# Optimization experiments

Measured on AMD Instinct MI355X. Metric: run time of the kernel, lower is better.

## Reference

```python
import jax, jax.numpy as jnp
import numpy as np

D_MODEL = 768
NUM_HEADS = 12
HEAD_DIM = D_MODEL // NUM_HEADS
SEQ = 4096
BATCH = 1


def setup_inputs() -> dict:
    key = jax.random.key(0)
    ks = jax.random.split(key, 6)
    scale = 1.0 / np.sqrt(D_MODEL)
    x = jax.random.normal(ks[0], (BATCH, SEQ, D_MODEL), dtype=jnp.float32)
    mask = jnp.tril(jnp.ones((SEQ, SEQ), dtype=bool))[None, None]  # [1,1,S,S] causal
    Wq = jax.random.normal(ks[1], (D_MODEL, D_MODEL), dtype=jnp.float32) * scale
    Wk = jax.random.normal(ks[2], (D_MODEL, D_MODEL), dtype=jnp.float32) * scale
    Wv = jax.random.normal(ks[3], (D_MODEL, D_MODEL), dtype=jnp.float32) * scale
    Wo = jax.random.normal(ks[4], (D_MODEL, D_MODEL), dtype=jnp.float32) * scale
    bo = jax.random.normal(ks[5], (D_MODEL,), dtype=jnp.float32) * 0.01
    return {"x": x, "mask": mask, "Wq": Wq, "Wk": Wk, "Wv": Wv, "Wo": Wo, "bo": bo}


def _rope_tables(seq_len, head_dim, dtype):
    # inv_freq over even dims; emb = cat(freqs, freqs) but only the first half
    # participates in the well-defined rotation (x1/x2 have head_dim//2 channels)
    inv_freq = 1.0 / (10000.0 ** (jnp.arange(0, head_dim, 2, dtype=dtype) / head_dim))
    t = jnp.arange(seq_len, dtype=dtype)
    freqs = t[:, None] * inv_freq[None, :]  # [S, head_dim//2]
    return jnp.cos(freqs), jnp.sin(freqs)


def _apply_rotary(xh, cos, sin):
    # xh: [B,H,S,hd]; cos/sin: [S, hd//2]
    x1 = xh[..., ::2]
    x2 = xh[..., 1::2]
    # faithful to source: concatenated (not interleaved) rotated halves
    return jnp.concatenate([x1 * cos - x2 * sin, x1 * sin + x2 * cos], axis=-1)


def reference(x, mask, Wq, Wk, Wv, Wo, bo):
    B, S, D = x.shape
    H, hd = NUM_HEADS, HEAD_DIM
    def split_heads(y):
        return y.reshape(B, S, H, hd).transpose(0, 2, 1, 3)  # [B,H,S,hd]
    q = split_heads(x @ Wq.T)
    k = split_heads(x @ Wk.T)
    v = split_heads(x @ Wv.T)
    cos, sin = _rope_tables(S, hd, x.dtype)
    q = _apply_rotary(q, cos, sin)
    k = _apply_rotary(k, cos, sin)
    scores = jnp.einsum('bhqd,bhkd->bhqk', q, k) / jnp.sqrt(jnp.asarray(hd, x.dtype))
    scores = jnp.where(mask, scores, jnp.asarray(-1e9, x.dtype))
    attn = jax.nn.softmax(scores, axis=-1)  # dropout is identity in eval
    out = jnp.einsum('bhqk,bhkd->bhqd', attn, v)
    out = out.transpose(0, 2, 1, 3).reshape(B, S, D)
    return out @ Wo.T + bo
```

## Files before the change

kernel.cpp:

```cpp
#include <hip/hip_runtime.h>
#include <hip/hip_bf16.h>
#include <math.h>

#define SEQ 4096
#define DM  768
#define NH  12
#define HD  64
#define PER ((size_t)NH * SEQ * HD)
#define XN  ((size_t)SEQ * DM)
#define WN  ((size_t)DM * DM)

typedef __attribute__((ext_vector_type(8))) short bf16x8;
typedef __attribute__((ext_vector_type(4))) short s16x4;
typedef __attribute__((ext_vector_type(4))) float f32x4;

#define MFMA(a, b, c) __builtin_amdgcn_mfma_f32_16x16x32_bf16((a), (b), (c), 0, 0, 0)

#if __has_builtin(__builtin_amdgcn_exp2f)
#define EXP2(x) __builtin_amdgcn_exp2f(x)
#else
#define EXP2(x) exp2f(x)
#endif

#define SWZ(row, blk) (((row) << 6) + ((((blk) ^ ((row) & 7))) << 3))

__device__ __forceinline__ unsigned short f2b(float f) {
    unsigned int u = __float_as_uint(f);
    u += 0x7FFFu + ((u >> 16) & 1u);
    return (unsigned short)(u >> 16);
}

__global__ __launch_bounds__(256) void prep_kernel(
    const float* __restrict__ x,  const float* __restrict__ wq,
    const float* __restrict__ wk, const float* __restrict__ wv,
    const float* __restrict__ wo,
    unsigned short* __restrict__ dstbase, float2* __restrict__ rope)
{
    const float* srcs[5] = {x, wq, wk, wv, wo};
    const size_t n4s[5]  = {XN / 4, WN / 4, WN / 4, WN / 4, WN / 4};
    unsigned short* d = dstbase;
    for (int rg = 0; rg < 5; ++rg) {
        const float4* s4 = (const float4*)srcs[rg];
        s16x4* d4 = (s16x4*)d;
        for (size_t i = (size_t)blockIdx.x * 256 + threadIdx.x; i < n4s[rg];
             i += (size_t)gridDim.x * 256) {
            const float4 v = s4[i];
            s16x4 p;
            p.x = (short)f2b(v.x); p.y = (short)f2b(v.y);
            p.z = (short)f2b(v.z); p.w = (short)f2b(v.w);
            d4[i] = p;
        }
        d += n4s[rg] * 4;
    }
    for (int g = blockIdx.x * 256 + threadIdx.x; g < 131072; g += gridDim.x * 256) {
        const int row = g >> 5, fi = g & 31;
        const float invf = expf(-(float)fi * 0.28782313662425576f);
        float sn, cs;
        sincosf((float)row * invf, &sn, &cs);
        rope[row * 32 + fi] = make_float2(cs, sn);
    }
}

__global__ __launch_bounds__(256) void qkv_mfma(
    const float* __restrict__ x,  const unsigned short* __restrict__ xb,
    const float* __restrict__ Wq, const float* __restrict__ Wk, const float* __restrict__ Wv,
    const unsigned short* __restrict__ Wqb, const unsigned short* __restrict__ Wkb,
    const unsigned short* __restrict__ Wvb,
    const float2* __restrict__ rope,
    unsigned short* __restrict__ Qo, unsigned short* __restrict__ Ko,
    unsigned short* __restrict__ Vo, int fast)
{
    __shared__ __align__(16) unsigned short Xs[2][4096];
    __shared__ __align__(16) unsigned short Ws[2][4096];
    __shared__ unsigned short VL[64 * 66];

    const int t    = threadIdx.x;
    const int w    = t >> 6;
    const int lane = t & 63;
    const int quad = lane >> 4;
    const int l16  = lane & 15;

    const int nt_b = blockIdx.y;
    const float* W; const unsigned short* Wb; int region;
    if (nt_b < 12)      { W = Wq; Wb = Wqb; region = 0; }
    else if (nt_b < 24) { W = Wk; Wb = Wkb; region = 1; }
    else                { W = Wv; Wb = Wvb; region = 2; }
    const int h  = nt_b % 12;
    const int s0 = blockIdx.x * 64;
    const int n0 = h * 64;

    f32x4 acc[4] = {{0,0,0,0},{0,0,0,0},{0,0,0,0},{0,0,0,0}};
    const int prow = t >> 3, pblk = t & 7;

    bf16x8 xr0, xr1, wr0, wr1;
    if (fast) {
        xr0 = *(const bf16x8*)&xb[(size_t)(s0 + prow) * DM + pblk * 8];
        xr1 = *(const bf16x8*)&xb[(size_t)(s0 + prow + 32) * DM + pblk * 8];
        wr0 = *(const bf16x8*)&Wb[(size_t)(n0 + prow) * DM + pblk * 8];
        wr1 = *(const bf16x8*)&Wb[(size_t)(n0 + prow + 32) * DM + pblk * 8];
        *(bf16x8*)&Xs[0][SWZ(prow, pblk)]      = xr0;
        *(bf16x8*)&Xs[0][SWZ(prow + 32, pblk)] = xr1;
        *(bf16x8*)&Ws[0][SWZ(prow, pblk)]      = wr0;
        *(bf16x8*)&Ws[0][SWZ(prow + 32, pblk)] = wr1;
    } else {
        for (int e = t; e < 1024; e += 256) {
            const int row = e >> 4, c4 = e & 15;
            const int off = SWZ(row, c4 >> 1) + (c4 & 1) * 4;
            const float4 xv = *(const float4*)&x[(size_t)(s0 + row) * DM + c4 * 4];
            s16x4 px; px.x = (short)f2b(xv.x); px.y = (short)f2b(xv.y);
            px.z = (short)f2b(xv.z); px.w = (short)f2b(xv.w);
            *(s16x4*)&Xs[0][off] = px;
            const float4 wv = *(const float4*)&W[(size_t)(n0 + row) * DM + c4 * 4];
            s16x4 pw; pw.x = (short)f2b(wv.x); pw.y = (short)f2b(wv.y);
            pw.z = (short)f2b(wv.z); pw.w = (short)f2b(wv.w);
            *(s16x4*)&Ws[0][off] = pw;
        }
    }
    __syncthreads();

    for (int kt = 0; kt < 12; ++kt) {
        const unsigned short* Xb  = Xs[kt & 1];
        const unsigned short* Wbt = Ws[kt & 1];
        if (fast && kt < 11) {
            const int k0 = (kt + 1) * 64;
            xr0 = *(const bf16x8*)&xb[(size_t)(s0 + prow) * DM + k0 + pblk * 8];
            xr1 = *(const bf16x8*)&xb[(size_t)(s0 + prow + 32) * DM + k0 + pblk * 8];
            wr0 = *(const bf16x8*)&Wb[(size_t)(n0 + prow) * DM + k0 + pblk * 8];
            wr1 = *(const bf16x8*)&Wb[(size_t)(n0 + prow + 32) * DM + k0 + pblk * 8];
        }
        const bf16x8 a0 = *(const bf16x8*)&Xb[SWZ(16 * w + l16, quad)];
        const bf16x8 a1 = *(const bf16x8*)&Xb[SWZ(16 * w + l16, 4 + quad)];
        #pragma unroll
        for (int nt = 0; nt < 4; ++nt) {
            const bf16x8 b0 = *(const bf16x8*)&Wbt[SWZ(16 * nt + l16, quad)];
            const bf16x8 b1 = *(const bf16x8*)&Wbt[SWZ(16 * nt + l16, 4 + quad)];
            acc[nt] = MFMA(a0, b0, acc[nt]);
            acc[nt] = MFMA(a1, b1, acc[nt]);
        }
        if (kt < 11) {
            const int nb = (kt + 1) & 1;
            if (fast) {
                *(bf16x8*)&Xs[nb][SWZ(prow, pblk)]      = xr0;
                *(bf16x8*)&Xs[nb][SWZ(prow + 32, pblk)] = xr1;
                *(bf16x8*)&Ws[nb][SWZ(prow, pblk)]      = wr0;
                *(bf16x8*)&Ws[nb][SWZ(prow + 32, pblk)] = wr1;
            } else {
                const int k0 = (kt + 1) * 64;
                for (int e = t; e < 1024; e += 256) {
                    const int row = e >> 4, c4 = e & 15;
                    const int off = SWZ(row, c4 >> 1) + (c4 & 1) * 4;
                    const float4 xv = *(const float4*)&x[(size_t)(s0 + row) * DM + k0 + c4 * 4];
                    s16x4 px; px.x = (short)f2b(xv.x); px.y = (short)f2b(xv.y);
                    px.z = (short)f2b(xv.z); px.w = (short)f2b(xv.w);
                    *(s16x4*)&Xs[nb][off] = px;
                    const float4 wv = *(const float4*)&W[(size_t)(n0 + row) * DM + k0 + c4 * 4];
                    s16x4 pw; pw.x = (short)f2b(wv.x); pw.y = (short)f2b(wv.y);
                    pw.z = (short)f2b(wv.z); pw.w = (short)f2b(wv.w);
                    *(s16x4*)&Ws[nb][off] = pw;
                }
            }
        }
        __syncthreads();
    }

    const size_t headoff = (size_t)h * SEQ * HD;
    if (region <= 1) {
        unsigned short* dst = (region == 0) ? Qo : Ko;
        const float qsc = (region == 0) ? 0.18033688011112042f : 1.0f;
        #pragma unroll
        for (int nt = 0; nt < 4; ++nt)
            #pragma unroll
            for (int r = 0; r < 4; ++r) {
                const int srow = s0 + 16 * w + quad * 4 + r;
                const int d  = nt * 16 + l16;
                const int fi = d >> 1;
                const float own = acc[nt][r] * qsc;
                const float oth = __shfl_xor(own, 1);
                float cs, sn;
                if (fast) {
                    const float2 t2 = rope[srow * 32 + fi];
                    cs = t2.x; sn = t2.y;
                } else {
                    const float invf = expf(-(float)fi * 0.28782313662425576f);
                    sincosf((float)srow * invf, &sn, &cs);
                }
                const float val = (d & 1) ? (oth * sn + own * cs)
                                          : (own * cs - oth * sn);
                dst[headoff + (size_t)srow * HD + ((d & 1) ? 32 : 0) + fi] = f2b(val);
            }
    } else {
        #pragma unroll
        for (int nt = 0; nt < 4; ++nt)
            #pragma unroll
            for (int r = 0; r < 4; ++r)
                VL[(nt * 16 + l16) * 66 + 16 * w + quad * 4 + r] = f2b(acc[nt][r]);
        __syncthreads();
        for (int e = t; e < 2048; e += 256) {
            const int d = e >> 5, sp = e & 31;
            const unsigned int v = (unsigned int)VL[d * 66 + 2 * sp] |
                                   ((unsigned int)VL[d * 66 + 2 * sp + 1] << 16);
            *(unsigned int*)&Vo[headoff + (size_t)d * SEQ + s0 + 2 * sp] = v;
        }
    }
}

__global__ __launch_bounds__(256, 2) void attn_mfma(
    const unsigned short* __restrict__ Q,
    const unsigned short* __restrict__ K,
    const unsigned short* __restrict__ V,
    unsigned short* __restrict__ O,
    float* __restrict__ Part)
{
    __shared__ __align__(16) unsigned char SM[53248];
    unsigned short* Kst = (unsigned short*)SM;
    unsigned short* Vt  = (unsigned short*)(SM + 16384);
    unsigned short* Ps  = (unsigned short*)(SM + 32768);
    float* ACC  = (float*)SM;
    float* ACC2 = (float*)(SM + 32768);
    float* Lx   = (float*)(SM + 51200);

    const int h  = blockIdx.y;
    const int xx = blockIdx.x;
    int i, kstart, nch, domask, partial, pslice;
    if (gridDim.x == 96) {
        if (xx < 64) {
            i = 63 - xx; kstart = 0;
            const int full = ((i * 64 + 63) >> 7) + 1;
            nch = full < 16 ? full : 16;
            domask  = (i <= 31);
            partial = (i >= 32); pslice = 0;
        } else {
            i = 127 - xx; kstart = 2048;
            nch = ((i * 64 + 63 - 2048) >> 7) + 1;
            domask = 1; partial = 1; pslice = 1;
        }
    } else {
        i = 63 - xx; kstart = 0;
        nch = ((i * 64 + 63) >> 7) + 1;
        domask = 1; partial = 0; pslice = 0;
    }
    const int q0 = i * 64;

    const int t    = threadIdx.x;
    const int w    = t >> 6;
    const int lane = t & 63;
    const int quad = lane >> 4;
    const int l16  = lane & 15;
    const size_t headoff = (size_t)h * SEQ * HD;

    for (int e = t; e < 512; e += 256) {
        const int row = e >> 3, bp = e & 7, blk = bp ^ (row & 7);
        *(bf16x8*)&Kst[row * 64 + bp * 8] =
            *(const bf16x8*)&Q[headoff + (size_t)(q0 + row) * HD + blk * 8];
    }
    __syncthreads();
    bf16x8 aQ[4][2];
    #pragma unroll
    for (int qt = 0; qt < 4; ++qt)
        #pragma unroll
        for (int hh = 0; hh < 2; ++hh)
            aQ[qt][hh] = *(const bf16x8*)&Kst[SWZ(16 * qt + l16, 4 * hh + quad)];
    __syncthreads();

    bf16x8 kreg[4], vreg[4];
    #pragma unroll
    for (int ii = 0; ii < 4; ++ii) {
        const int e = t + ii * 256, row = e >> 3, bp = e & 7, blk = bp ^ (row & 7);
        kreg[ii] = *(const bf16x8*)&K[headoff + (size_t)(kstart + row) * HD + blk * 8];
    }
    #pragma unroll
    for (int ii = 0; ii < 4; ++ii) {
        const int e = t + ii * 256, row = e >> 4, bp = e & 15, blk = bp ^ (row & 15);
        vreg[ii] = *(const bf16x8*)&V[headoff + (size_t)row * SEQ + kstart + blk * 8];
    }
    #pragma unroll
    for (int ii = 0; ii < 4; ++ii) {
        const int e = t + ii * 256, row = e >> 3, bp = e & 7;
        *(bf16x8*)&Kst[row * 64 + bp * 8] = kreg[ii];
    }
    #pragma unroll
    for (int ii = 0; ii < 4; ++ii) {
        const int e = t + ii * 256, row = e >> 4, bp = e & 15;
        *(bf16x8*)&Vt[row * 128 + bp * 8] = vreg[ii];
    }
    __syncthreads();

    bf16x8 ones;
    #pragma unroll
    for (int ii = 0; ii < 8; ++ii) ones[ii] = (short)0x3F80;

    f32x4 oT[4][4];
    #pragma unroll
    for (int dt = 0; dt < 4; ++dt)
        #pragma unroll
        for (int qt = 0; qt < 4; ++qt) oT[dt][qt] = (f32x4){0,0,0,0};
    f32x4 lT[4] = {{0,0,0,0},{0,0,0,0},{0,0,0,0},{0,0,0,0}};

    unsigned short* usp = Ps + w * 2560;

    for (int c = 0; c < nch; ++c) {
        const int k0 = kstart + c * 128;

        f32x4 sC[4][2];
        #pragma unroll
        for (int qt = 0; qt < 4; ++qt)
            #pragma unroll
            for (int kt = 0; kt < 2; ++kt) sC[qt][kt] = (f32x4){0,0,0,0};
        #pragma unroll
        for (int kt = 0; kt < 2; ++kt) {
            const int krow = 32 * w + 16 * kt + l16;
            #pragma unroll
            for (int hh = 0; hh < 2; ++hh) {
                const bf16x8 bK = *(const bf16x8*)&Kst[SWZ(krow, 4 * hh + quad)];
                #pragma unroll
                for (int qt = 0; qt < 4; ++qt)
                    sC[qt][kt] = MFMA(aQ[qt][hh], bK, sC[qt][kt]);
            }
        }

        if (c < nch - 1) {
            const int kn = k0 + 128;
            #pragma unroll
            for (int ii = 0; ii < 4; ++ii) {
                const int e = t + ii * 256, row = e >> 3, bp = e & 7, blk = bp ^ (row & 7);
                kreg[ii] = *(const bf16x8*)&K[headoff + (size_t)(kn + row) * HD + blk * 8];
            }
            #pragma unroll
            for (int ii = 0; ii < 4; ++ii) {
                const int e = t + ii * 256, row = e >> 4, bp = e & 15, blk = bp ^ (row & 15);
                vreg[ii] = *(const bf16x8*)&V[headoff + (size_t)row * SEQ + kn + blk * 8];
            }
        }

        if (domask && c == nch - 1) {
            #pragma unroll
            for (int kt = 0; kt < 2; ++kt) {
                const int key = k0 + 32 * w + 16 * kt + l16;
                #pragma unroll
                for (int qt = 0; qt < 4; ++qt)
                    #pragma unroll
                    for (int r = 0; r < 4; ++r)
                        if (key > q0 + 16 * qt + 4 * quad + r) sC[qt][kt][r] = -1e30f;
            }
        }

        #pragma unroll
        for (int qt = 0; qt < 4; ++qt)
            #pragma unroll
            for (int kt = 0; kt < 2; ++kt)
                #pragma unroll
                for (int r = 0; r < 4; ++r)
                    usp[(16 * qt + 4 * quad + r) * 40 + 16 * kt + l16] =
                        f2b(EXP2(sC[qt][kt][r]));
        asm volatile("s_waitcnt lgkmcnt(0)" ::: "memory");

        bf16x8 aV[4];
        #pragma unroll
        for (int dt = 0; dt < 4; ++dt) {
            const int row = 16 * dt + l16;
            aV[dt] = *(const bf16x8*)&Vt[row * 128 + (((4 * w + quad) ^ (row & 15)) << 3)];
        }
        #pragma unroll
        for (int qt = 0; qt < 4; ++qt) {
            const bf16x8 bP = *(const bf16x8*)&usp[(16 * qt + l16) * 40 + quad * 8];
            lT[qt] = MFMA(ones, bP, lT[qt]);
            #pragma unroll
            for (int dt = 0; dt < 4; ++dt)
                oT[dt][qt] = MFMA(aV[dt], bP, oT[dt][qt]);
        }

        __syncthreads();
        if (c < nch - 1) {
            #pragma unroll
            for (int ii = 0; ii < 4; ++ii) {
                const int e = t + ii * 256, row = e >> 3, bp = e & 7;
                *(bf16x8*)&Kst[row * 64 + bp * 8] = kreg[ii];
            }
            #pragma unroll
            for (int ii = 0; ii < 4; ++ii) {
                const int e = t + ii * 256, row = e >> 4, bp = e & 15;
                *(bf16x8*)&Vt[row * 128 + bp * 8] = vreg[ii];
            }
        }
        __syncthreads();
    }

    if (w != 0 && quad == 0) {
        #pragma unroll
        for (int qt = 0; qt < 4; ++qt)
            Lx[w * 64 + 16 * qt + l16] = lT[qt][0];
    }
    if (w == 1) {
        #pragma unroll
        for (int dt = 0; dt < 4; ++dt)
            #pragma unroll
            for (int qt = 0; qt < 4; ++qt)
                *(f32x4*)&ACC[(16 * qt + l16) * 72 + 16 * dt + 4 * quad] = oT[dt][qt];
    }
    __syncthreads();
    if (w == 0) {
        #pragma unroll
        for (int dt = 0; dt < 4; ++dt)
            #pragma unroll
            for (int qt = 0; qt < 4; ++qt)
                oT[dt][qt] += *(const f32x4*)&ACC[(16 * qt + l16) * 72 + 16 * dt + 4 * quad];
    }
    if (w == 2) {
        #pragma unroll
        for (int dt = 0; dt < 4; ++dt)
            #pragma unroll
            for (int qt = 0; qt < 4; ++qt)
                *(f32x4*)&ACC2[(16 * qt + l16) * 72 + 16 * dt + 4 * quad] = oT[dt][qt];
    }
    __syncthreads();
    if (w == 0) {
        #pragma unroll
        for (int dt = 0; dt < 4; ++dt)
            #pragma unroll
            for (int qt = 0; qt < 4; ++qt)
                oT[dt][qt] += *(const f32x4*)&ACC2[(16 * qt + l16) * 72 + 16 * dt + 4 * quad];
    }
    if (w == 3) {
        #pragma unroll
        for (int dt = 0; dt < 4; ++dt)
            #pragma unroll
            for (int qt = 0; qt < 4; ++qt)
                *(f32x4*)&ACC[(16 * qt + l16) * 72 + 16 * dt + 4 * quad] = oT[dt][qt];
    }
    __syncthreads();
    if (w == 0) {
        float ls[4];
        #pragma unroll
        for (int qt = 0; qt < 4; ++qt) {
            #pragma unroll
            for (int dt = 0; dt < 4; ++dt)
                oT[dt][qt] += *(const f32x4*)&ACC[(16 * qt + l16) * 72 + 16 * dt + 4 * quad];
            ls[qt] = lT[qt][0] + Lx[64 + 16 * qt + l16] +
                     Lx[128 + 16 * qt + l16] + Lx[192 + 16 * qt + l16];
        }
        if (!partial) {
            #pragma unroll
            for (int qt = 0; qt < 4; ++qt) {
                const float inv = 1.0f / ls[qt];
                const size_t rowoff = (size_t)(q0 + 16 * qt + l16) * DM + h * HD;
                #pragma unroll
                for (int dt = 0; dt < 4; ++dt) {
                    ushort4 u;
                    u.x = f2b(oT[dt][qt][0] * inv);
                    u.y = f2b(oT[dt][qt][1] * inv);
                    u.z = f2b(oT[dt][qt][2] * inv);
                    u.w = f2b(oT[dt][qt][3] * inv);
                    *(ushort4*)&O[rowoff + 16 * dt + 4 * quad] = u;
                }
            }
        } else {
            float* P = Part + (size_t)(((i - 32) * 12 + h) * 2 + pslice) * 4160;
            #pragma unroll
            for (int dt = 0; dt < 4; ++dt)
                #pragma unroll
                for (int qt = 0; qt < 4; ++qt)
                    *(f32x4*)&P[(16 * qt + l16) * 64 + 16 * dt + 4 * quad] = oT[dt][qt];
            if (quad == 0) {
                #pragma unroll
                for (int qt = 0; qt < 4; ++qt)
                    P[4096 + 16 * qt + l16] = ls[qt];
            }
        }
    }
}

__global__ __launch_bounds__(256) void reduce_attn(
    const float* __restrict__ Part, unsigned short* __restrict__ O)
{
    const int b  = blockIdx.x;
    const int i  = 32 + b / 12, h = b % 12;
    const int q0 = i * 64;
    const float* P0 = Part + (size_t)(b * 2 + 0) * 4160;
    const float* P1 = Part + (size_t)(b * 2 + 1) * 4160;
    __shared__ float linv[64];
    const int t = threadIdx.x;
    if (t < 64) linv[t] = 1.0f / (P0[4096 + t] + P1[4096 + t]);
    __syncthreads();
    for (int idx = t; idx < 4096; idx += 256) {
        const int q = idx >> 6, d = idx & 63;
        const float v = (P0[q * 64 + d] + P1[q * 64 + d]) * linv[q];
        O[(size_t)(q0 + q) * DM + h * HD + d] = f2b(v);
    }
}

__global__ __launch_bounds__(256) void proj_mfma(
    const unsigned short* __restrict__ A,
    const float* __restrict__ Wo, const unsigned short* __restrict__ Wob,
    const float* __restrict__ bo,
    float* __restrict__ out, int fast)
{
    __shared__ __align__(16) unsigned short Xs[2][4096];
    __shared__ __align__(16) unsigned short Ws[2][4096];

    const int t    = threadIdx.x;
    const int w    = t >> 6;
    const int lane = t & 63;
    const int quad = lane >> 4;
    const int l16  = lane & 15;
    const int s0 = blockIdx.x * 64;
    const int n0 = blockIdx.y * 64;
    const int prow = t >> 3, pblk = t & 7;

    f32x4 acc[4] = {{0,0,0,0},{0,0,0,0},{0,0,0,0},{0,0,0,0}};

    bf16x8 ar0, ar1, wr0, wr1;
    ar0 = *(const bf16x8*)&A[(size_t)(s0 + prow) * DM + pblk * 8];
    ar1 = *(const bf16x8*)&A[(size_t)(s0 + prow + 32) * DM + pblk * 8];
    *(bf16x8*)&Xs[0][SWZ(prow, pblk)]      = ar0;
    *(bf16x8*)&Xs[0][SWZ(prow + 32, pblk)] = ar1;
    if (fast) {
        wr0 = *(const bf16x8*)&Wob[(size_t)(n0 + prow) * DM + pblk * 8];
        wr1 = *(const bf16x8*)&Wob[(size_t)(n0 + prow + 32) * DM + pblk * 8];
        *(bf16x8*)&Ws[0][SWZ(prow, pblk)]      = wr0;
        *(bf16x8*)&Ws[0][SWZ(prow + 32, pblk)] = wr1;
    } else {
        for (int e = t; e < 1024; e += 256) {
            const int row = e >> 4, c4 = e & 15;
            const float4 wv = *(const float4*)&Wo[(size_t)(n0 + row) * DM + c4 * 4];
            s16x4 pw; pw.x = (short)f2b(wv.x); pw.y = (short)f2b(wv.y);
            pw.z = (short)f2b(wv.z); pw.w = (short)f2b(wv.w);
            *(s16x4*)&Ws[0][SWZ(row, c4 >> 1) + (c4 & 1) * 4] = pw;
        }
    }
    __syncthreads();

    for (int kt = 0; kt < 12; ++kt) {
        const unsigned short* Xb  = Xs[kt & 1];
        const unsigned short* Wbt = Ws[kt & 1];
        if (kt < 11) {
            const int k0 = (kt + 1) * 64;
            ar0 = *(const bf16x8*)&A[(size_t)(s0 + prow) * DM + k0 + pblk * 8];
            ar1 = *(const bf16x8*)&A[(size_t)(s0 + prow + 32) * DM + k0 + pblk * 8];
            if (fast) {
                wr0 = *(const bf16x8*)&Wob[(size_t)(n0 + prow) * DM + k0 + pblk * 8];
                wr1 = *(const bf16x8*)&Wob[(size_t)(n0 + prow + 32) * DM + k0 + pblk * 8];
            }
        }
        const bf16x8 a0 = *(const bf16x8*)&Xb[SWZ(16 * w + l16, quad)];
        const bf16x8 a1 = *(const bf16x8*)&Xb[SWZ(16 * w + l16, 4 + quad)];
        #pragma unroll
        for (int nt = 0; nt < 4; ++nt) {
            const bf16x8 b0 = *(const bf16x8*)&Wbt[SWZ(16 * nt + l16, quad)];
            const bf16x8 b1 = *(const bf16x8*)&Wbt[SWZ(16 * nt + l16, 4 + quad)];
            acc[nt] = MFMA(a0, b0, acc[nt]);
            acc[nt] = MFMA(a1, b1, acc[nt]);
        }
        if (kt < 11) {
            const int nb = (kt + 1) & 1;
            *(bf16x8*)&Xs[nb][SWZ(prow, pblk)]      = ar0;
            *(bf16x8*)&Xs[nb][SWZ(prow + 32, pblk)] = ar1;
            if (fast) {
                *(bf16x8*)&Ws[nb][SWZ(prow, pblk)]      = wr0;
                *(bf16x8*)&Ws[nb][SWZ(prow + 32, pblk)] = wr1;
            } else {
                const int k0 = (kt + 1) * 64;
                for (int e = t; e < 1024; e += 256) {
                    const int row = e >> 4, c4 = e & 15;
                    const float4 wv = *(const float4*)&Wo[(size_t)(n0 + row) * DM + k0 + c4 * 4];
                    s16x4 pw; pw.x = (short)f2b(wv.x); pw.y = (short)f2b(wv.y);
                    pw.z = (short)f2b(wv.z); pw.w = (short)f2b(wv.w);
                    *(s16x4*)&Ws[nb][SWZ(row, c4 >> 1) + (c4 & 1) * 4] = pw;
                }
            }
        }
        __syncthreads();
    }

    #pragma unroll
    for (int nt = 0; nt < 4; ++nt)
        #pragma unroll
        for (int r = 0; r < 4; ++r) {
            const int srow = s0 + 16 * w + quad * 4 + r;
            const int n    = n0 + nt * 16 + l16;
            out[(size_t)srow * DM + n] = acc[nt][r] + bo[n];
        }
}

extern "C" void kernel_launch(void* const* d_in, const int* in_sizes, int n_in,
                              void* d_out, int out_size, void* d_ws, size_t ws_size,
                              hipStream_t stream) {
    const float* x  = (const float*)d_in[0];
    const float* Wq = (const float*)d_in[2];
    const float* Wk = (const float*)d_in[3];
    const float* Wv = (const float*)d_in[4];
    const float* Wo = (const float*)d_in[5];
    const float* bo = (const float*)d_in[6];
    float* out = (float*)d_out;

    unsigned short* U  = (unsigned short*)d_ws;
    unsigned short* Qw = U;
    unsigned short* Kw = U + PER;
    unsigned short* Vw = U + 2 * PER;
    unsigned short* Ow = U + 3 * PER;
    unsigned short* xb  = U + 4 * PER;
    unsigned short* Wqb = xb + XN;
    unsigned short* Wkb = Wqb + WN;
    unsigned short* Wvb = Wkb + WN;
    unsigned short* Wob = Wvb + WN;
    float2* rope = (float2*)(Wob + WN);
    float*  part = (float*)(rope + 4096 * 32);
    const size_t need  = (char*)part - (char*)d_ws;
    const size_t need2 = need + (size_t)384 * 2 * 4160 * 4;
    const int fast  = (ws_size >= need)  ? 1 : 0;
    const int split = (ws_size >= need2) ? 1 : 0;

    if (fast)
        prep_kernel<<<1024, 256, 0, stream>>>(x, Wq, Wk, Wv, Wo, xb, rope);
    qkv_mfma<<<dim3(SEQ / 64, 36), 256, 0, stream>>>(
        x, xb, Wq, Wk, Wv, Wqb, Wkb, Wvb, rope, Qw, Kw, Vw, fast);
    if (split) {
        attn_mfma<<<dim3(96, NH), 256, 0, stream>>>(Qw, Kw, Vw, Ow, part);
        reduce_attn<<<dim3(384), 256, 0, stream>>>(part, Ow);
    } else {
        attn_mfma<<<dim3(64, NH), 256, 0, stream>>>(Qw, Kw, Vw, Ow, part);
    }
    proj_mfma<<<dim3(SEQ / 64, DM / 64), 256, 0, stream>>>(Ow, Wo, Wob, bo, out, fast);
}
```

Baseline: 243.3 us.

## Enlarge QKV and output-projection GEMM tiles to 128x128 per block

Both GEMM kernels move from 64x64 output tiles, where each warp owns a 16x64 strip, to 128x128 tiles where each warp computes a 64x64 sub-tile with a 4x4 grid of MFMA accumulators. Each fragment loaded from shared memory is now reused across four MFMAs, which raises arithmetic intensity and cuts LDS and global traffic per FLOP. The swizzle is moved to the global-load address so the shared-memory stores become linear. The V transpose epilogue is widened to match the larger tile. In exchange the grids shrink, to 576 blocks for QKV and 192 for the projection, and the kernels use more registers and 64KB of LDS, which may reduce occupancy and leave CUs underused in the projection.

```diff
diff --git a/kernel.cpp b/kernel.cpp
--- a/kernel.cpp
+++ b/kernel.cpp
@@ -61,7 +61,7 @@
     }
 }
 
-__global__ __launch_bounds__(256) void qkv_mfma(
+__global__ __launch_bounds__(256) void qkv128(
     const float* __restrict__ x,  const unsigned short* __restrict__ xb,
     const float* __restrict__ Wq, const float* __restrict__ Wk, const float* __restrict__ Wv,
     const unsigned short* __restrict__ Wqb, const unsigned short* __restrict__ Wkb,
@@ -70,136 +70,165 @@
     unsigned short* __restrict__ Qo, unsigned short* __restrict__ Ko,
     unsigned short* __restrict__ Vo, int fast)
 {
-    __shared__ __align__(16) unsigned short Xs[2][4096];
-    __shared__ __align__(16) unsigned short Ws[2][4096];
-    __shared__ unsigned short VL[64 * 66];
+    __shared__ __align__(16) unsigned short SMEM[32768];
+    unsigned short* At0 = SMEM;
+    unsigned short* At1 = SMEM + 8192;
+    unsigned short* Bt0 = SMEM + 16384;
+    unsigned short* Bt1 = SMEM + 24576;
 
     const int t    = threadIdx.x;
     const int w    = t >> 6;
     const int lane = t & 63;
     const int quad = lane >> 4;
     const int l16  = lane & 15;
-
-    const int nt_b = blockIdx.y;
-    const float* W; const unsigned short* Wb; int region;
-    if (nt_b < 12)      { W = Wq; Wb = Wqb; region = 0; }
-    else if (nt_b < 24) { W = Wk; Wb = Wkb; region = 1; }
-    else                { W = Wv; Wb = Wvb; region = 2; }
-    const int h  = nt_b % 12;
-    const int s0 = blockIdx.x * 64;
-    const int n0 = h * 64;
-
-    f32x4 acc[4] = {{0,0,0,0},{0,0,0,0},{0,0,0,0},{0,0,0,0}};
-    const int prow = t >> 3, pblk = t & 7;
-
-    bf16x8 xr0, xr1, wr0, wr1;
+    const int region = blockIdx.y / 6;
+    const int ntile  = blockIdx.y % 6;
+    const int n0 = ntile * 128;
+    const int s0 = blockIdx.x * 128;
+    const int m0  = 64 * (w & 1);
+    const int nn0 = 64 * (w >> 1);
+
+    const unsigned short* Wb = (region == 0) ? Wqb : (region == 1) ? Wkb : Wvb;
+    const float*          Wf = (region == 0) ? Wq  : (region == 1) ? Wk  : Wv;
+
+    f32x4 acc[4][4];
+    #pragma unroll
+    for (int i = 0; i < 4; ++i)
+        #pragma unroll
+        for (int j = 0; j < 4; ++j) acc[i][j] = (f32x4){0, 0, 0, 0};
+
+    bf16x8 areg[4], breg[4];
     if (fast) {
-        xr0 = *(const bf16x8*)&xb[(size_t)(s0 + prow) * DM + pblk * 8];
-        xr1 = *(const bf16x8*)&xb[(size_t)(s0 + prow + 32) * DM + pblk * 8];
-        wr0 = *(const bf16x8*)&Wb[(size_t)(n0 + prow) * DM + pblk * 8];
-        wr1 = *(const bf16x8*)&Wb[(size_t)(n0 + prow + 32) * DM + pblk * 8];
-        *(bf16x8*)&Xs[0][SWZ(prow, pblk)]      = xr0;
-        *(bf16x8*)&Xs[0][SWZ(prow + 32, pblk)] = xr1;
-        *(bf16x8*)&Ws[0][SWZ(prow, pblk)]      = wr0;
-        *(bf16x8*)&Ws[0][SWZ(prow + 32, pblk)] = wr1;
+        #pragma unroll
+        for (int i = 0; i < 4; ++i) {
+            const int s = t + i * 256, row = s >> 3, bp = s & 7, blk = bp ^ (row & 7);
+            areg[i] = *(const bf16x8*)&xb[(size_t)(s0 + row) * DM + blk * 8];
+            breg[i] = *(const bf16x8*)&Wb[(size_t)(n0 + row) * DM + blk * 8];
+        }
+        #pragma unroll
+        for (int i = 0; i < 4; ++i) {
+            const int s = t + i * 256, row = s >> 3, bp = s & 7;
+            *(bf16x8*)&At0[row * 64 + bp * 8] = areg[i];
+            *(bf16x8*)&Bt0[row * 64 + bp * 8] = breg[i];
+        }
     } else {
-        for (int e = t; e < 1024; e += 256) {
+        for (int e = t; e < 2048; e += 256) {
             const int row = e >> 4, c4 = e & 15;
-            const int off = SWZ(row, c4 >> 1) + (c4 & 1) * 4;
+            const int off = (row << 6) + (((c4 >> 1) ^ (row & 7)) << 3) + (c4 & 1) * 4;
             const float4 xv = *(const float4*)&x[(size_t)(s0 + row) * DM + c4 * 4];
             s16x4 px; px.x = (short)f2b(xv.x); px.y = (short)f2b(xv.y);
             px.z = (short)f2b(xv.z); px.w = (short)f2b(xv.w);
-            *(s16x4*)&Xs[0][off] = px;
-            const float4 wv = *(const float4*)&W[(size_t)(n0 + row) * DM + c4 * 4];
+            *(s16x4*)&At0[off] = px;
+            const float4 wv = *(const float4*)&Wf[(size_t)(n0 + row) * DM + c4 * 4];
             s16x4 pw; pw.x = (short)f2b(wv.x); pw.y = (short)f2b(wv.y);
             pw.z = (short)f2b(wv.z); pw.w = (short)f2b(wv.w);
-            *(s16x4*)&Ws[0][off] = pw;
+            *(s16x4*)&Bt0[off] = pw;
         }
     }
     __syncthreads();
 
     for (int kt = 0; kt < 12; ++kt) {
-        const unsigned short* Xb  = Xs[kt & 1];
-        const unsigned short* Wbt = Ws[kt & 1];
         if (fast && kt < 11) {
-            const int k0 = (kt + 1) * 64;
-            xr0 = *(const bf16x8*)&xb[(size_t)(s0 + prow) * DM + k0 + pblk * 8];
-            xr1 = *(const bf16x8*)&xb[(size_t)(s0 + prow + 32) * DM + k0 + pblk * 8];
-            wr0 = *(const bf16x8*)&Wb[(size_t)(n0 + prow) * DM + k0 + pblk * 8];
-            wr1 = *(const bf16x8*)&Wb[(size_t)(n0 + prow + 32) * DM + k0 + pblk * 8];
-        }
-        const bf16x8 a0 = *(const bf16x8*)&Xb[SWZ(16 * w + l16, quad)];
-        const bf16x8 a1 = *(const bf16x8*)&Xb[SWZ(16 * w + l16, 4 + quad)];
-        #pragma unroll
-        for (int nt = 0; nt < 4; ++nt) {
-            const bf16x8 b0 = *(const bf16x8*)&Wbt[SWZ(16 * nt + l16, quad)];
-            const bf16x8 b1 = *(const bf16x8*)&Wbt[SWZ(16 * nt + l16, 4 + quad)];
-            acc[nt] = MFMA(a0, b0, acc[nt]);
-            acc[nt] = MFMA(a1, b1, acc[nt]);
-        }
+            const int k0n = (kt + 1) * 64;
+            #pragma unroll
+            for (int i = 0; i < 4; ++i) {
+                const int s = t + i * 256, row = s >> 3, bp = s & 7, blk = bp ^ (row & 7);
+                areg[i] = *(const bf16x8*)&xb[(size_t)(s0 + row) * DM + k0n + blk * 8];
+                breg[i] = *(const bf16x8*)&Wb[(size_t)(n0 + row) * DM + k0n + blk * 8];
+            }
+        }
+        const unsigned short* Ab = (kt & 1) ? At1 : At0;
+        const unsigned short* Bb = (kt & 1) ? Bt1 : Bt0;
+
+        bf16x8 aA[4][2], bB[4][2];
+        #pragma unroll
+        for (int i = 0; i < 4; ++i)
+            #pragma unroll
+            for (int hh = 0; hh < 2; ++hh) {
+                aA[i][hh] = *(const bf16x8*)&Ab[SWZ(m0 + 16 * i + l16, 4 * hh + quad)];
+                bB[i][hh] = *(const bf16x8*)&Bb[SWZ(nn0 + 16 * i + l16, 4 * hh + quad)];
+            }
+        #pragma unroll
+        for (int hh = 0; hh < 2; ++hh)
+            #pragma unroll
+            for (int i = 0; i < 4; ++i)
+                #pragma unroll
+                for (int j = 0; j < 4; ++j)
+                    acc[i][j] = MFMA(aA[i][hh], bB[j][hh], acc[i][j]);
+
         if (kt < 11) {
-            const int nb = (kt + 1) & 1;
+            unsigned short* An = ((kt + 1) & 1) ? At1 : At0;
+            unsigned short* Bn = ((kt + 1) & 1) ? Bt1 : Bt0;
             if (fast) {
-                *(bf16x8*)&Xs[nb][SWZ(prow, pblk)]      = xr0;
-                *(bf16x8*)&Xs[nb][SWZ(prow + 32, pblk)] = xr1;
-                *(bf16x8*)&Ws[nb][SWZ(prow, pblk)]      = wr0;
-                *(bf16x8*)&Ws[nb][SWZ(prow + 32, pblk)] = wr1;
+                #pragma unroll
+                for (int i = 0; i < 4; ++i) {
+                    const int s = t + i * 256, row = s >> 3, bp = s & 7;
+                    *(bf16x8*)&An[row * 64 + bp * 8] = areg[i];
+                    *(bf16x8*)&Bn[row * 64 + bp * 8] = breg[i];
+                }
             } else {
-                const int k0 = (kt + 1) * 64;
-                for (int e = t; e < 1024; e += 256) {
+                const int k0n = (kt + 1) * 64;
+                for (int e = t; e < 2048; e += 256) {
                     const int row = e >> 4, c4 = e & 15;
-                    const int off = SWZ(row, c4 >> 1) + (c4 & 1) * 4;
-                    const float4 xv = *(const float4*)&x[(size_t)(s0 + row) * DM + k0 + c4 * 4];
+                    const int off = (row << 6) + (((c4 >> 1) ^ (row & 7)) << 3) + (c4 & 1) * 4;
+                    const float4 xv = *(const float4*)&x[(size_t)(s0 + row) * DM + k0n + c4 * 4];
                     s16x4 px; px.x = (short)f2b(xv.x); px.y = (short)f2b(xv.y);
                     px.z = (short)f2b(xv.z); px.w = (short)f2b(xv.w);
-                    *(s16x4*)&Xs[nb][off] = px;
-                    const float4 wv = *(const float4*)&W[(size_t)(n0 + row) * DM + k0 + c4 * 4];
+                    *(s16x4*)&An[off] = px;
+                    const float4 wv = *(const float4*)&Wf[(size_t)(n0 + row) * DM + k0n + c4 * 4];
                     s16x4 pw; pw.x = (short)f2b(wv.x); pw.y = (short)f2b(wv.y);
                     pw.z = (short)f2b(wv.z); pw.w = (short)f2b(wv.w);
-                    *(s16x4*)&Ws[nb][off] = pw;
+                    *(s16x4*)&Bn[off] = pw;
                 }
             }
         }
         __syncthreads();
     }
 
-    const size_t headoff = (size_t)h * SEQ * HD;
     if (region <= 1) {
         unsigned short* dst = (region == 0) ? Qo : Ko;
         const float qsc = (region == 0) ? 0.18033688011112042f : 1.0f;
         #pragma unroll
-        for (int nt = 0; nt < 4; ++nt)
-            #pragma unroll
-            for (int r = 0; r < 4; ++r) {
-                const int srow = s0 + 16 * w + quad * 4 + r;
-                const int d  = nt * 16 + l16;
-                const int fi = d >> 1;
-                const float own = acc[nt][r] * qsc;
-                const float oth = __shfl_xor(own, 1);
-                float cs, sn;
-                if (fast) {
-                    const float2 t2 = rope[srow * 32 + fi];
-                    cs = t2.x; sn = t2.y;
-                } else {
-                    const float invf = expf(-(float)fi * 0.28782313662425576f);
-                    sincosf((float)srow * invf, &sn, &cs);
+        for (int i = 0; i < 4; ++i)
+            #pragma unroll
+            for (int j = 0; j < 4; ++j)
+                #pragma unroll
+                for (int r = 0; r < 4; ++r) {
+                    const int srow = s0 + m0 + 16 * i + 4 * quad + r;
+                    const int n = n0 + nn0 + 16 * j + l16;
+                    const int h = n >> 6, d = n & 63, fi = d >> 1;
+                    const float own = acc[i][j][r] * qsc;
+                    const float oth = __shfl_xor(own, 1);
+                    float cs, sn;
+                    if (fast) {
+                        const float2 t2 = rope[srow * 32 + fi];
+                        cs = t2.x; sn = t2.y;
+                    } else {
+                        const float invf = expf(-(float)fi * 0.28782313662425576f);
+                        sincosf((float)srow * invf, &sn, &cs);
+                    }
+                    const float val = (d & 1) ? (oth * sn + own * cs)
+                                              : (own * cs - oth * sn);
+                    dst[(size_t)h * SEQ * HD + (size_t)srow * HD +
+                        ((d & 1) ? 32 : 0) + fi] = f2b(val);
                 }
-                const float val = (d & 1) ? (oth * sn + own * cs)
-                                          : (own * cs - oth * sn);
-                dst[headoff + (size_t)srow * HD + ((d & 1) ? 32 : 0) + fi] = f2b(val);
-            }
     } else {
-        #pragma unroll
-        for (int nt = 0; nt < 4; ++nt)
-            #pragma unroll
-            for (int r = 0; r < 4; ++r)
-                VL[(nt * 16 + l16) * 66 + 16 * w + quad * 4 + r] = f2b(acc[nt][r]);
+        unsigned short* VL = SMEM;
+        #pragma unroll
+        for (int i = 0; i < 4; ++i)
+            #pragma unroll
+            for (int j = 0; j < 4; ++j)
+                #pragma unroll
+                for (int r = 0; r < 4; ++r)
+                    VL[(nn0 + 16 * j + l16) * 130 + m0 + 16 * i + 4 * quad + r] =
+                        f2b(acc[i][j][r]);
         __syncthreads();
-        for (int e = t; e < 2048; e += 256) {
-            const int d = e >> 5, sp = e & 31;
-            const unsigned int v = (unsigned int)VL[d * 66 + 2 * sp] |
-                                   ((unsigned int)VL[d * 66 + 2 * sp + 1] << 16);
-            *(unsigned int*)&Vo[headoff + (size_t)d * SEQ + s0 + 2 * sp] = v;
+        for (int e = t; e < 8192; e += 256) {
+            const int dl = e >> 6, sp = e & 63;
+            const unsigned int v = (unsigned int)VL[dl * 130 + 2 * sp] |
+                                   ((unsigned int)VL[dl * 130 + 2 * sp + 1] << 16);
+            const int n = n0 + dl, h = n >> 6, d = n & 63;
+            *(unsigned int*)&Vo[(size_t)h * SEQ * HD + (size_t)d * SEQ + s0 + 2 * sp] = v;
         }
     }
 }
@@ -488,83 +517,106 @@
     }
 }
 
-__global__ __launch_bounds__(256) void proj_mfma(
+__global__ __launch_bounds__(256) void proj128(
     const unsigned short* __restrict__ A,
     const float* __restrict__ Wo, const unsigned short* __restrict__ Wob,
     const float* __restrict__ bo,
     float* __restrict__ out, int fast)
 {
-    __shared__ __align__(16) unsigned short Xs[2][4096];
-    __shared__ __align__(16) unsigned short Ws[2][4096];
+    __shared__ __align__(16) unsigned short SMEM[32768];
+    unsigned short* At0 = SMEM;
+    unsigned short* At1 = SMEM + 8192;
+    unsigned short* Bt0 = SMEM + 16384;
+    unsigned short* Bt1 = SMEM + 24576;
 
     const int t    = threadIdx.x;
     const int w    = t >> 6;
     const int lane = t & 63;
     const int quad = lane >> 4;
     const int l16  = lane & 15;
-    const int s0 = blockIdx.x * 64;
-    const int n0 = blockIdx.y * 64;
-    const int prow = t >> 3, pblk = t & 7;
-
-    f32x4 acc[4] = {{0,0,0,0},{0,0,0,0},{0,0,0,0},{0,0,0,0}};
-
-    bf16x8 ar0, ar1, wr0, wr1;
-    ar0 = *(const bf16x8*)&A[(size_t)(s0 + prow) * DM + pblk * 8];
-    ar1 = *(const bf16x8*)&A[(size_t)(s0 + prow + 32) * DM + pblk * 8];
-    *(bf16x8*)&Xs[0][SWZ(prow, pblk)]      = ar0;
-    *(bf16x8*)&Xs[0][SWZ(prow + 32, pblk)] = ar1;
-    if (fast) {
-        wr0 = *(const bf16x8*)&Wob[(size_t)(n0 + prow) * DM + pblk * 8];
-        wr1 = *(const bf16x8*)&Wob[(size_t)(n0 + prow + 32) * DM + pblk * 8];
-        *(bf16x8*)&Ws[0][SWZ(prow, pblk)]      = wr0;
-        *(bf16x8*)&Ws[0][SWZ(prow + 32, pblk)] = wr1;
-    } else {
-        for (int e = t; e < 1024; e += 256) {
+    const int s0 = blockIdx.x * 128;
+    const int n0 = blockIdx.y * 128;
+    const int m0  = 64 * (w & 1);
+    const int nn0 = 64 * (w >> 1);
+
+    f32x4 acc[4][4];
+    #pragma unroll
+    for (int i = 0; i < 4; ++i)
+        #pragma unroll
+        for (int j = 0; j < 4; ++j) acc[i][j] = (f32x4){0, 0, 0, 0};
+
+    bf16x8 areg[4], breg[4];
+    #pragma unroll
+    for (int i = 0; i < 4; ++i) {
+        const int s = t + i * 256, row = s >> 3, bp = s & 7, blk = bp ^ (row & 7);
+        areg[i] = *(const bf16x8*)&A[(size_t)(s0 + row) * DM + blk * 8];
+        if (fast) breg[i] = *(const bf16x8*)&Wob[(size_t)(n0 + row) * DM + blk * 8];
+    }
+    #pragma unroll
+    for (int i = 0; i < 4; ++i) {
+        const int s = t + i * 256, row = s >> 3, bp = s & 7;
+        *(bf16x8*)&At0[row * 64 + bp * 8] = areg[i];
+        if (fast) *(bf16x8*)&Bt0[row * 64 + bp * 8] = breg[i];
+    }
+    if (!fast) {
+        for (int e = t; e < 2048; e += 256) {
             const int row = e >> 4, c4 = e & 15;
+            const int off = (row << 6) + (((c4 >> 1) ^ (row & 7)) << 3) + (c4 & 1) * 4;
             const float4 wv = *(const float4*)&Wo[(size_t)(n0 + row) * DM + c4 * 4];
             s16x4 pw; pw.x = (short)f2b(wv.x); pw.y = (short)f2b(wv.y);
             pw.z = (short)f2b(wv.z); pw.w = (short)f2b(wv.w);
-            *(s16x4*)&Ws[0][SWZ(row, c4 >> 1) + (c4 & 1) * 4] = pw;
+            *(s16x4*)&Bt0[off] = pw;
         }
     }
     __syncthreads();
 
     for (int kt = 0; kt < 12; ++kt) {
-        const unsigned short* Xb  = Xs[kt & 1];
-        const unsigned short* Wbt = Ws[kt & 1];
         if (kt < 11) {
-            const int k0 = (kt + 1) * 64;
-            ar0 = *(const bf16x8*)&A[(size_t)(s0 + prow) * DM + k0 + pblk * 8];
-            ar1 = *(const bf16x8*)&A[(size_t)(s0 + prow + 32) * DM + k0 + pblk * 8];
-            if (fast) {
-                wr0 = *(const bf16x8*)&Wob[(size_t)(n0 + prow) * DM + k0 + pblk * 8];
-                wr1 = *(const bf16x8*)&Wob[(size_t)(n0 + prow + 32) * DM + k0 + pblk * 8];
-            }
-        }
-        const bf16x8 a0 = *(const bf16x8*)&Xb[SWZ(16 * w + l16, quad)];
-        const bf16x8 a1 = *(const bf16x8*)&Xb[SWZ(16 * w + l16, 4 + quad)];
-        #pragma unroll
-        for (int nt = 0; nt < 4; ++nt) {
-            const bf16x8 b0 = *(const bf16x8*)&Wbt[SWZ(16 * nt + l16, quad)];
-            const bf16x8 b1 = *(const bf16x8*)&Wbt[SWZ(16 * nt + l16, 4 + quad)];
-            acc[nt] = MFMA(a0, b0, acc[nt]);
-            acc[nt] = MFMA(a1, b1, acc[nt]);
-        }
+            const int k0n = (kt + 1) * 64;
+            #pragma unroll
+            for (int i = 0; i < 4; ++i) {
+                const int s = t + i * 256, row = s >> 3, bp = s & 7, blk = bp ^ (row & 7);
+                areg[i] = *(const bf16x8*)&A[(size_t)(s0 + row) * DM + k0n + blk * 8];
+                if (fast) breg[i] = *(const bf16x8*)&Wob[(size_t)(n0 + row) * DM + k0n + blk * 8];
+            }
+        }
+        const unsigned short* Ab = (kt & 1) ? At1 : At0;
+        const unsigned short* Bb = (kt & 1) ? Bt1 : Bt0;
+
+        bf16x8 aA[4][2], bB[4][2];
+        #pragma unroll
+        for (int i = 0; i < 4; ++i)
+            #pragma unroll
+            for (int hh = 0; hh < 2; ++hh) {
+                aA[i][hh] = *(const bf16x8*)&Ab[SWZ(m0 + 16 * i + l16, 4 * hh + quad)];
+                bB[i][hh] = *(const bf16x8*)&Bb[SWZ(nn0 + 16 * i + l16, 4 * hh + quad)];
+            }
+        #pragma unroll
+        for (int hh = 0; hh < 2; ++hh)
+            #pragma unroll
+            for (int i = 0; i < 4; ++i)
+                #pragma unroll
+                for (int j = 0; j < 4; ++j)
+                    acc[i][j] = MFMA(aA[i][hh], bB[j][hh], acc[i][j]);
+
         if (kt < 11) {
-            const int nb = (kt + 1) & 1;
-            *(bf16x8*)&Xs[nb][SWZ(prow, pblk)]      = ar0;
-            *(bf16x8*)&Xs[nb][SWZ(prow + 32, pblk)] = ar1;
-            if (fast) {
-                *(bf16x8*)&Ws[nb][SWZ(prow, pblk)]      = wr0;
-                *(bf16x8*)&Ws[nb][SWZ(prow + 32, pblk)] = wr1;
-            } else {
-                const int k0 = (kt + 1) * 64;
-                for (int e = t; e < 1024; e += 256) {
+            unsigned short* An = ((kt + 1) & 1) ? At1 : At0;
+            unsigned short* Bn = ((kt + 1) & 1) ? Bt1 : Bt0;
+            #pragma unroll
+            for (int i = 0; i < 4; ++i) {
+                const int s = t + i * 256, row = s >> 3, bp = s & 7;
+                *(bf16x8*)&An[row * 64 + bp * 8] = areg[i];
+                if (fast) *(bf16x8*)&Bn[row * 64 + bp * 8] = breg[i];
+            }
+            if (!fast) {
+                const int k0n = (kt + 1) * 64;
+                for (int e = t; e < 2048; e += 256) {
                     const int row = e >> 4, c4 = e & 15;
-                    const float4 wv = *(const float4*)&Wo[(size_t)(n0 + row) * DM + k0 + c4 * 4];
+                    const int off = (row << 6) + (((c4 >> 1) ^ (row & 7)) << 3) + (c4 & 1) * 4;
+                    const float4 wv = *(const float4*)&Wo[(size_t)(n0 + row) * DM + k0n + c4 * 4];
                     s16x4 pw; pw.x = (short)f2b(wv.x); pw.y = (short)f2b(wv.y);
                     pw.z = (short)f2b(wv.z); pw.w = (short)f2b(wv.w);
-                    *(s16x4*)&Ws[nb][SWZ(row, c4 >> 1) + (c4 & 1) * 4] = pw;
+                    *(s16x4*)&Bn[off] = pw;
                 }
             }
         }
@@ -572,12 +624,16 @@
     }
 
     #pragma unroll
-    for (int nt = 0; nt < 4; ++nt)
-        #pragma unroll
-        for (int r = 0; r < 4; ++r) {
-            const int srow = s0 + 16 * w + quad * 4 + r;
-            const int n    = n0 + nt * 16 + l16;
-            out[(size_t)srow * DM + n] = acc[nt][r] + bo[n];
+    for (int i = 0; i < 4; ++i)
+        #pragma unroll
+        for (int j = 0; j < 4; ++j) {
+            const int n = n0 + nn0 + 16 * j + l16;
+            const float bv = bo[n];
+            #pragma unroll
+            for (int r = 0; r < 4; ++r) {
+                const int srow = s0 + m0 + 16 * i + 4 * quad + r;
+                out[(size_t)srow * DM + n] = acc[i][j][r] + bv;
+            }
         }
 }
 
@@ -611,7 +667,7 @@
 
     if (fast)
         prep_kernel<<<1024, 256, 0, stream>>>(x, Wq, Wk, Wv, Wo, xb, rope);
-    qkv_mfma<<<dim3(SEQ / 64, 36), 256, 0, stream>>>(
+    qkv128<<<dim3(SEQ / 128, 18), 256, 0, stream>>>(
         x, xb, Wq, Wk, Wv, Wqb, Wkb, Wvb, rope, Qw, Kw, Vw, fast);
     if (split) {
         attn_mfma<<<dim3(96, NH), 256, 0, stream>>>(Qw, Kw, Vw, Ow, part);
@@ -619,5 +675,5 @@
     } else {
         attn_mfma<<<dim3(64, NH), 256, 0, stream>>>(Qw, Kw, Vw, Ow, part);
     }
-    proj_mfma<<<dim3(SEQ / 64, DM / 64), 256, 0, stream>>>(Ow, Wo, Wob, bo, out, fast);
+    proj128<<<dim3(SEQ / 128, DM / 128), 256, 0, stream>>>(Ow, Wo, Wob, bo, out, fast);
 }
```

After: 246.5 us. Within noise of the previous version (+1.3%).
